# Kernel optimization log

Hardware: AMD Instinct MI355X
Metric: run time of the kernel (lower is better)

Reference implementation:

```python
import jax, jax.numpy as jnp
import numpy as np

B, T_ENC, U = 8, 200, 100
VOCAB, ENC_DIM, PRED_DIM, EMBED_DIM = 1024, 512, 512, 128


def setup_inputs() -> dict:
    key = jax.random.key(0)
    ks = jax.random.split(key, 13)
    n = lambda k, shape, fan_in: (jax.random.normal(k, shape, jnp.float32) / np.sqrt(fan_in)).astype(jnp.float32)
    return {
        "enc_out": jax.random.normal(ks[0], (B, T_ENC, ENC_DIM), jnp.float32),
        "targets": jax.random.randint(ks[1], (B, U), 0, VOCAB, jnp.int32),
        "target_len": jnp.full((B,), U, jnp.int32),
        # params
        "emb_table": n(ks[2], (VOCAB + 1, EMBED_DIM), 1.0),
        "W_ih": n(ks[3], (4 * PRED_DIM, EMBED_DIM), EMBED_DIM),
        "W_hh": n(ks[4], (4 * PRED_DIM, PRED_DIM), PRED_DIM),
        "b_ih": jnp.zeros((4 * PRED_DIM,), jnp.float32),
        "b_hh": jnp.zeros((4 * PRED_DIM,), jnp.float32),
        "W_enc": n(ks[5], (PRED_DIM, ENC_DIM), ENC_DIM),
        "b_enc": jnp.zeros((PRED_DIM,), jnp.float32),
        "W_pred": n(ks[6], (PRED_DIM, PRED_DIM), PRED_DIM),
        "b_pred": jnp.zeros((PRED_DIM,), jnp.float32),
        "W_joint": n(ks[7], (VOCAB + 1, PRED_DIM), PRED_DIM),
        "b_joint": jnp.zeros((VOCAB + 1,), jnp.float32),
    }


def reference(enc_out, targets, target_len, emb_table, W_ih, W_hh, b_ih, b_hh,
              W_enc, b_enc, W_pred, b_pred, W_joint, b_joint):
    # targets_with_blank: prepend blank_id = vocab_size
    blank_id = emb_table.shape[0] - 1
    Bsz = targets.shape[0]
    tw = jnp.concatenate([jnp.full((Bsz, 1), blank_id, targets.dtype), targets], axis=1)
    emb = emb_table[tw]  # (B, U+1, E)

    P = W_hh.shape[1]
    h0 = jnp.zeros((Bsz, P), emb.dtype)

    def lstm_step(carry, x_t):
        h, c = carry
        gates = x_t @ W_ih.T + b_ih + h @ W_hh.T + b_hh  # (B, 4P)
        i, f, g, o = jnp.split(gates, 4, axis=-1)  # PyTorch LSTMCell gate order
        i, f, o = jax.nn.sigmoid(i), jax.nn.sigmoid(f), jax.nn.sigmoid(o)
        c = f * c + i * jnp.tanh(g)
        h = o * jnp.tanh(c)
        return (h, c), h

    _, pred = jax.lax.scan(lstm_step, (h0, h0), jnp.swapaxes(emb, 0, 1))
    pred = jnp.swapaxes(pred, 0, 1)  # (B, U+1, P)

    f_enc = enc_out @ W_enc.T + b_enc   # (B, T, P)
    f_pred = pred @ W_pred.T + b_pred   # (B, U+1, P)
    joint = jnp.tanh(f_enc[:, :, None, :] + f_pred[:, None, :, :])  # (B, T, U+1, P)
    logits = joint @ W_joint.T + b_joint  # (B, T, U+1, V+1)
    return logits
```

## Files before the change

kernel.cpp:

```cpp
#include <hip/hip_runtime.h>
#include <stdint.h>
#include <stddef.h>

#define BB 8
#define TENC 200
#define UU 100
#define UP1 101
#define VP1 1025
#define ED 128
#define PD 512
#define LSTM_NWG 64

typedef __attribute__((ext_vector_type(8))) unsigned short ushort8;
typedef __attribute__((ext_vector_type(8))) __bf16 bf16x8;
typedef __attribute__((ext_vector_type(4))) float f32x4;

__device__ __forceinline__ float bf2f(unsigned short u){
  unsigned int x = ((unsigned int)u) << 16;
  return __builtin_bit_cast(float, x);
}
__device__ __forceinline__ unsigned short f2bf(float f){
  unsigned int x = __builtin_bit_cast(unsigned int, f);
  unsigned int r = (x + 0x7fffu + ((x >> 16) & 1u)) >> 16;
  return (unsigned short)r;
}
__device__ __forceinline__ float tanh_fast(float x){
  float e = __expf(2.0f * x);
  return 1.0f - 2.0f / (e + 1.0f);
}
__device__ __forceinline__ float sigm(float x){
  return 1.0f / (1.0f + __expf(-x));
}
__device__ __forceinline__ void gload_lds16(const unsigned short* gsrc, unsigned short* ldst){
  __builtin_amdgcn_global_load_lds((const __attribute__((address_space(1))) void*)gsrc,
                                   (__attribute__((address_space(3))) void*)ldst, 16, 0, 0);
}

__global__ __launch_bounds__(256) void k_cvt_bf16(const float* __restrict__ src,
                                                  unsigned short* __restrict__ dst, int n){
  int i = blockIdx.x * 256 + threadIdx.x;
  if (i < n) dst[i] = f2bf(src[i]);
}

__global__ __launch_bounds__(256) void k_xgate(
    const float* __restrict__ emb, const int* __restrict__ targets,
    const float* __restrict__ W_ih, const float* __restrict__ b_ih,
    const float* __restrict__ b_hh, float* __restrict__ xg)
{
  __shared__ float e_s[BB * ED];
  const int u  = blockIdx.x >> 2;
  const int jq = blockIdx.x & 3;
  const int tid = threadIdx.x;
  for (int idx = tid; idx < BB * ED; idx += 256){
    int b = idx >> 7, e = idx & 127;
    int tok = (u == 0) ? 1024 : targets[b * UU + (u - 1)];
    e_s[idx] = emb[(size_t)tok * ED + e];
  }
  __syncthreads();
  float acc[2][BB];
  #pragma unroll
  for (int r = 0; r < 2; r++)
    #pragma unroll
    for (int b = 0; b < BB; b++) acc[r][b] = 0.0f;
  const int j0 = jq * 512 + tid;
  const float* w0p = W_ih + (size_t)j0 * ED;
  const float* w1p = W_ih + (size_t)(j0 + 256) * ED;
  for (int e = 0; e < ED; e++){
    float w0 = w0p[e], w1 = w1p[e];
    #pragma unroll
    for (int b = 0; b < BB; b++){
      float ev = e_s[b * ED + e];
      acc[0][b] = fmaf(ev, w0, acc[0][b]);
      acc[1][b] = fmaf(ev, w1, acc[1][b]);
    }
  }
  #pragma unroll
  for (int r = 0; r < 2; r++){
    int j = j0 + r * 256;
    float bias = b_ih[j] + b_hh[j];
    #pragma unroll
    for (int b = 0; b < BB; b++)
      xg[((size_t)b * UP1 + u) * 2048 + j] = acc[r][b] + bias;
  }
}

__global__ __launch_bounds__(256) void k_lstm_all(
    const float* __restrict__ xg, const float* __restrict__ W_hh,
    float* __restrict__ pred, unsigned int* __restrict__ cnt)
{
  __shared__ float h_s[8][520];
  __shared__ float red[32 * 257];
  __shared__ float gates_s[32][9];
  const int tid = threadIdx.x;
  const int wg  = blockIdx.x;
  const int p0  = wg * 8;
  const int jg = tid >> 5, kc = tid & 31;
  const float* wrow[4];
  #pragma unroll
  for (int r = 0; r < 4; r++){
    int jl = jg * 4 + r;
    int grow = (jl >> 3) * PD + p0 + (jl & 7);
    wrow[r] = W_hh + (size_t)grow * PD;
  }
  float c_reg = 0.0f;
  for (int u = 0; u < UP1; u++){
    float xi = 0.f, xf = 0.f, xgv = 0.f, xo = 0.f;
    if (tid < 64){
      int pl = tid >> 3, b = tid & 7;
      const float* xr = xg + ((size_t)(b * UP1 + u)) * 2048;
      int p = p0 + pl;
      xi = xr[p]; xf = xr[512 + p]; xgv = xr[1024 + p]; xo = xr[1536 + p];
    }
    if (u > 0){
      if (tid == 0){
        while (__hip_atomic_load(&cnt[u - 1], __ATOMIC_RELAXED, __HIP_MEMORY_SCOPE_AGENT) < LSTM_NWG)
          __builtin_amdgcn_s_sleep(8);
      }
      __syncthreads();
      float tmp[16];
      #pragma unroll
      for (int j = 0; j < 16; j++){
        int i = tid + 256 * j;
        int b2 = i >> 9, k = i & 511;
        tmp[j] = __hip_atomic_load(pred + ((size_t)(b2 * UP1 + (u - 1))) * PD + k,
                                   __ATOMIC_RELAXED, __HIP_MEMORY_SCOPE_AGENT);
      }
      #pragma unroll
      for (int j = 0; j < 16; j++){
        int i = tid + 256 * j;
        h_s[i >> 9][i & 511] = tmp[j];
      }
    } else {
      for (int i = tid; i < 8 * PD; i += 256) h_s[i >> 9][i & 511] = 0.0f;
    }
    __syncthreads();
    float acc[4][BB];
    #pragma unroll
    for (int r = 0; r < 4; r++)
      #pragma unroll
      for (int b = 0; b < BB; b++) acc[r][b] = 0.0f;
    for (int i = 0; i < 16; i++){
      int k = kc + 32 * i;
      float hv[BB];
      #pragma unroll
      for (int b = 0; b < BB; b++) hv[b] = h_s[b][k];
      #pragma unroll
      for (int r = 0; r < 4; r++){
        float wv = wrow[r][k];
        #pragma unroll
        for (int b = 0; b < BB; b++) acc[r][b] = fmaf(hv[b], wv, acc[r][b]);
      }
    }
    #pragma unroll
    for (int r = 0; r < 4; r++)
      #pragma unroll
      for (int b = 0; b < BB; b++)
        red[kc * 257 + jg * 32 + r * 8 + b] = acc[r][b];
    __syncthreads();
    {
      int jl = tid >> 3, b = tid & 7;
      float s = 0.0f;
      #pragma unroll
      for (int kk = 0; kk < 32; kk++)
        s += red[kk * 257 + (jl >> 2) * 32 + (jl & 3) * 8 + b];
      gates_s[jl][b] = s;
    }
    __syncthreads();
    if (tid < 64){
      int pl = tid >> 3, b = tid & 7;
      int p = p0 + pl;
      float gi = gates_s[0  + pl][b] + xi;
      float gf = gates_s[8  + pl][b] + xf;
      float gg = gates_s[16 + pl][b] + xgv;
      float go = gates_s[24 + pl][b] + xo;
      float iv = sigm(gi), fv = sigm(gf), ov = sigm(go);
      c_reg = fv * c_reg + iv * tanh_fast(gg);
      float hval = ov * tanh_fast(c_reg);
      __hip_atomic_store(pred + ((size_t)(b * UP1 + u)) * PD + p, hval,
                         __ATOMIC_RELAXED, __HIP_MEMORY_SCOPE_AGENT);
    }
    if (u < UP1 - 1){
      if (tid == 0){
        asm volatile("s_waitcnt vmcnt(0)" ::: "memory");
        __hip_atomic_fetch_add(&cnt[u], 1u, __ATOMIC_RELAXED, __HIP_MEMORY_SCOPE_AGENT);
      }
    }
  }
}

__global__ __launch_bounds__(256) void k_gemm_bias_bf16(
    const float* __restrict__ A, const float* __restrict__ W,
    const float* __restrict__ bias, unsigned short* __restrict__ out, int M)
{
  __shared__ float a_s[16][68];
  __shared__ float b_s[16][68];
  const int m0 = blockIdx.x * 64, n0 = blockIdx.y * 64;
  const int tid = threadIdx.x;
  const int tx = tid & 15, ty = tid >> 4;
  float acc[4][4];
  #pragma unroll
  for (int i2 = 0; i2 < 4; i2++)
    #pragma unroll
    for (int j2 = 0; j2 < 4; j2++) acc[i2][j2] = 0.0f;
  for (int k0 = 0; k0 < 512; k0 += 16){
    int mm = tid >> 2, k4 = (tid & 3) * 4;
    int row = m0 + mm; if (row >= M) row = M - 1;
    float4 av = *(const float4*)(A + (size_t)row * 512 + k0 + k4);
    a_s[k4 + 0][mm] = av.x; a_s[k4 + 1][mm] = av.y;
    a_s[k4 + 2][mm] = av.z; a_s[k4 + 3][mm] = av.w;
    float4 bv = *(const float4*)(W + (size_t)(n0 + mm) * 512 + k0 + k4);
    b_s[k4 + 0][mm] = bv.x; b_s[k4 + 1][mm] = bv.y;
    b_s[k4 + 2][mm] = bv.z; b_s[k4 + 3][mm] = bv.w;
    __syncthreads();
    #pragma unroll
    for (int k = 0; k < 16; k++){
      float4 a4 = *(const float4*)&a_s[k][ty * 4];
      float4 b4 = *(const float4*)&b_s[k][tx * 4];
      float aa[4] = {a4.x, a4.y, a4.z, a4.w};
      float bb[4] = {b4.x, b4.y, b4.z, b4.w};
      #pragma unroll
      for (int i2 = 0; i2 < 4; i2++)
        #pragma unroll
        for (int j2 = 0; j2 < 4; j2++)
          acc[i2][j2] = fmaf(aa[i2], bb[j2], acc[i2][j2]);
    }
    __syncthreads();
  }
  #pragma unroll
  for (int i2 = 0; i2 < 4; i2++){
    int m = m0 + ty * 4 + i2;
    if (m < M){
      #pragma unroll
      for (int j2 = 0; j2 < 4; j2++){
        int n = n0 + tx * 4 + j2;
        out[(size_t)m * 512 + n] = f2bf(acc[i2][j2] + bias[n]);
      }
    }
  }
}

__global__ __launch_bounds__(512, 1) void k_joint3(
    const unsigned short* __restrict__ fe, const unsigned short* __restrict__ fp,
    const unsigned short* __restrict__ wj, const float* __restrict__ bj,
    float* __restrict__ out)
{
  __shared__ unsigned short A_s[128 * 512];
  __shared__ unsigned short B_s[3][128 * 32];
  const int tu = blockIdx.x;
  const int b  = blockIdx.y;
  const int tt = tu / 13, ut = tu - tt * 13;
  const int t0 = tt * 16, u0 = ut * 8;
  const int tid = threadIdx.x;
  const int w = tid >> 6, l = tid & 63;
  const int l15 = l & 15, lg = l >> 4;
  const int wr = w >> 1, wc = w & 1;

  auto issue = [&](int idx){
    int nt = idx >> 4, ks = idx & 15;
    int rb = tid >> 2, cs = tid & 3;
    int col8 = cs ^ ((rb >> 1) & 3);
    const unsigned short* src = wj + (size_t)(nt * 128 + rb) * 512 + ks * 32 + col8 * 8;
    gload_lds16(src, (unsigned short*)B_s[idx % 3] + (size_t)(w * 64) * 8);
  };

  issue(0);

  for (int rr = 0; rr < 16; rr++){
    int row = rr * 8 + w;
    int ti = row >> 3, ui = row & 7;
    int t = t0 + ti, uu = u0 + ui;
    ushort8 a = {0,0,0,0,0,0,0,0};
    if (t < TENC && uu < UP1){
      ushort8 f8 = *(const ushort8*)(fe + (size_t)(b * TENC + t) * 512 + l * 8);
      ushort8 p8 = *(const ushort8*)(fp + (size_t)(b * UP1 + uu) * 512 + l * 8);
      #pragma unroll
      for (int j = 0; j < 8; j++)
        a[j] = f2bf(tanh_fast(bf2f(f8[j]) + bf2f(p8[j])));
    }
    int byteo = row * 1024 + ((l * 16) ^ ((row & 7) << 4));
    *(ushort8*)((char*)A_s + byteo) = a;
  }
  __syncthreads();

  f32x4 acc[2][4];
  #pragma unroll
  for (int fr = 0; fr < 2; fr++)
    #pragma unroll
    for (int fc = 0; fc < 4; fc++)
      acc[fr][fc] = (f32x4){0.f, 0.f, 0.f, 0.f};

  for (int idx = 0; idx < 128; idx++){
    const int nt = idx >> 4, ks = idx & 15;
    if (idx + 1 < 128){
      issue(idx + 1);
      asm volatile("s_waitcnt vmcnt(1)" ::: "memory");
    } else {
      asm volatile("s_waitcnt vmcnt(0)" ::: "memory");
    }
    __builtin_amdgcn_s_barrier();

    const unsigned short* bb = (const unsigned short*)B_s[idx % 3];
    bf16x8 bfr[4], afr[2];
    #pragma unroll
    for (int fc = 0; fc < 4; fc++){
      int rb = wc * 64 + fc * 16 + l15;
      int byteo = rb * 64 + ((lg ^ ((rb >> 1) & 3)) * 16);
      bfr[fc] = __builtin_bit_cast(bf16x8, *(const ushort8*)((const char*)bb + byteo));
    }
    #pragma unroll
    for (int fr = 0; fr < 2; fr++){
      int ra = wr * 32 + fr * 16 + l15;
      int k8 = ks * 4 + lg;
      int byteo = ra * 1024 + ((k8 * 16) ^ ((ra & 7) << 4));
      afr[fr] = __builtin_bit_cast(bf16x8, *(const ushort8*)((const char*)A_s + byteo));
    }
    #pragma unroll
    for (int fr = 0; fr < 2; fr++)
      #pragma unroll
      for (int fc = 0; fc < 4; fc++)
        acc[fr][fc] = __builtin_amdgcn_mfma_f32_16x16x32_bf16(bfr[fc], afr[fr], acc[fr][fc], 0, 0, 0);

    if (ks == 15){
      #pragma unroll
      for (int fr = 0; fr < 2; fr++){
        int m = wr * 32 + fr * 16 + l15;
        int t = t0 + (m >> 3), uu2 = u0 + (m & 7);
        if (t < TENC && uu2 < UP1){
          float* orow = out + ((size_t)(b * TENC + t) * UP1 + uu2) * VP1;
          #pragma unroll
          for (int fc = 0; fc < 4; fc++){
            int nb = nt * 128 + wc * 64 + fc * 16 + lg * 4;
            float4 bv = *(const float4*)(bj + nb);
            f32x4 v = acc[fr][fc];
            float4 st = {v[0] + bv.x, v[1] + bv.y, v[2] + bv.z, v[3] + bv.w};
            *(float4*)(orow + nb) = st;
          }
        }
        #pragma unroll
        for (int fc = 0; fc < 4; fc++)
          acc[fr][fc] = (f32x4){0.f, 0.f, 0.f, 0.f};
      }
    }
  }

  {
    int row = tid >> 2, q = tid & 3;
    float s = 0.0f;
    const unsigned short* w1 = wj + (size_t)1024 * 512;
    #pragma unroll 4
    for (int j = 0; j < 16; j++){
      int k8 = q * 16 + j;
      int byteo = row * 1024 + ((k8 * 16) ^ ((row & 7) << 4));
      ushort8 a8 = *(const ushort8*)((const char*)A_s + byteo);
      ushort8 w8 = *(const ushort8*)(w1 + k8 * 8);
      #pragma unroll
      for (int jj = 0; jj < 8; jj++)
        s += bf2f(a8[jj]) * bf2f(w8[jj]);
    }
    s += __shfl_xor(s, 1);
    s += __shfl_xor(s, 2);
    if (q == 0){
      int t = t0 + (row >> 3), uu = u0 + (row & 7);
      if (t < TENC && uu < UP1)
        out[((size_t)(b * TENC + t) * UP1 + uu) * VP1 + 1024] = s + bj[1024];
    }
  }
}

extern "C" void kernel_launch(void* const* d_in, const int* in_sizes, int n_in,
                              void* d_out, int out_size, void* d_ws, size_t ws_size,
                              hipStream_t stream) {
  const float* enc_out = (const float*)d_in[0];
  const int*   targets = (const int*)d_in[1];
  const float* emb     = (const float*)d_in[3];
  const float* W_ih    = (const float*)d_in[4];
  const float* W_hh    = (const float*)d_in[5];
  const float* b_ih    = (const float*)d_in[6];
  const float* b_hh    = (const float*)d_in[7];
  const float* W_enc   = (const float*)d_in[8];
  const float* b_enc   = (const float*)d_in[9];
  const float* W_pred  = (const float*)d_in[10];
  const float* b_pred  = (const float*)d_in[11];
  const float* W_joint = (const float*)d_in[12];
  const float* b_joint = (const float*)d_in[13];
  float* out = (float*)d_out;

  char* ws = (char*)d_ws;
  float* xg            = (float*)(ws + 0);
  float* pred          = (float*)(ws + 6619136);
  unsigned short* feb  = (unsigned short*)(ws + 8273920);
  unsigned short* fpb  = (unsigned short*)(ws + 9912320);
  unsigned short* wjb  = (unsigned short*)(ws + 10739712);
  unsigned int*   cnt  = (unsigned int*)(ws + 11789312);

  hipMemsetAsync(cnt, 0, UP1 * sizeof(unsigned int), stream);
  hipLaunchKernelGGL(k_cvt_bf16, dim3((VP1 * 512 + 255) / 256), dim3(256), 0, stream,
                     W_joint, wjb, VP1 * 512);
  hipLaunchKernelGGL(k_xgate, dim3(404), dim3(256), 0, stream,
                     emb, targets, W_ih, b_ih, b_hh, xg);
  hipLaunchKernelGGL(k_gemm_bias_bf16, dim3(25, 8), dim3(256), 0, stream,
                     enc_out, W_enc, b_enc, feb, 1600);
  hipLaunchKernelGGL(k_lstm_all, dim3(LSTM_NWG), dim3(256), 0, stream,
                     xg, W_hh, pred, cnt);
  hipLaunchKernelGGL(k_gemm_bias_bf16, dim3(13, 8), dim3(256), 0, stream,
                     pred, W_pred, b_pred, fpb, 808);
  hipLaunchKernelGGL(k_joint3, dim3(169, 8), dim3(512), 0, stream,
                     feb, fpb, wjb, b_joint, out);
}
```

Before: 1.004 ms.

## Cache LSTM weights in LDS, per-WG flag sync, deeper joint prefetch, nontemporal stores

The persistent LSTM kernel now loads its W_hh slice into LDS once and computes each gate/batch dot product per thread, which removes the cross-thread reduction. Grid sync changes from one shared atomic counter to per-workgroup sequence flags polled by a wavefront. The hidden state is exchanged through a small double-buffered array read with cache-bypassing loads. The joint GEMM prefetches two B tiles ahead with a single barrier per step and writes logits with nontemporal stores. The added LDS use and the more aggressive polling could raise occupancy or contention costs.

```diff
diff --git a/kernel.cpp b/kernel.cpp
--- a/kernel.cpp
+++ b/kernel.cpp
@@ -86,104 +86,90 @@
 
 __global__ __launch_bounds__(256) void k_lstm_all(
     const float* __restrict__ xg, const float* __restrict__ W_hh,
-    float* __restrict__ pred, unsigned int* __restrict__ cnt)
+    float* __restrict__ pred, float* __restrict__ hb, unsigned int* __restrict__ seq)
 {
+  __shared__ float W_s[32][520];
   __shared__ float h_s[8][520];
-  __shared__ float red[32 * 257];
-  __shared__ float gates_s[32][9];
+  __shared__ float gates_s[32][8];
   const int tid = threadIdx.x;
   const int wg  = blockIdx.x;
   const int p0  = wg * 8;
-  const int jg = tid >> 5, kc = tid & 31;
-  const float* wrow[4];
-  #pragma unroll
-  for (int r = 0; r < 4; r++){
-    int jl = jg * 4 + r;
-    int grow = (jl >> 3) * PD + p0 + (jl & 7);
-    wrow[r] = W_hh + (size_t)grow * PD;
+  const int row = tid >> 3, bb = tid & 7;
+  {
+    int r = tid >> 3;
+    int grow = (r >> 3) * PD + p0 + (r & 7);
+    const float* src = W_hh + (size_t)grow * PD;
+    for (int c = (tid & 7); c < 128; c += 8)
+      *(float4*)&W_s[r][c * 4] = *(const float4*)(src + c * 4);
   }
   float c_reg = 0.0f;
+  __syncthreads();
   for (int u = 0; u < UP1; u++){
-    float xi = 0.f, xf = 0.f, xgv = 0.f, xo = 0.f;
-    if (tid < 64){
-      int pl = tid >> 3, b = tid & 7;
-      const float* xr = xg + ((size_t)(b * UP1 + u)) * 2048;
-      int p = p0 + pl;
-      xi = xr[p]; xf = xr[512 + p]; xgv = xr[1024 + p]; xo = xr[1536 + p];
-    }
+    float xv = xg[((size_t)(bb * UP1 + u)) * 2048 + (row >> 3) * 512 + p0 + (row & 7)];
     if (u > 0){
-      if (tid == 0){
-        while (__hip_atomic_load(&cnt[u - 1], __ATOMIC_RELAXED, __HIP_MEMORY_SCOPE_AGENT) < LSTM_NWG)
-          __builtin_amdgcn_s_sleep(8);
+      if (tid < 64){
+        while (1){
+          unsigned int v = __hip_atomic_load(&seq[tid], __ATOMIC_RELAXED, __HIP_MEMORY_SCOPE_AGENT);
+          if (__all(v >= (unsigned int)u)) break;
+          __builtin_amdgcn_s_sleep(1);
+        }
       }
       __syncthreads();
-      float tmp[16];
-      #pragma unroll
-      for (int j = 0; j < 16; j++){
-        int i = tid + 256 * j;
-        int b2 = i >> 9, k = i & 511;
-        tmp[j] = __hip_atomic_load(pred + ((size_t)(b2 * UP1 + (u - 1))) * PD + k,
-                                   __ATOMIC_RELAXED, __HIP_MEMORY_SCOPE_AGENT);
-      }
-      #pragma unroll
-      for (int j = 0; j < 16; j++){
-        int i = tid + 256 * j;
-        h_s[i >> 9][i & 511] = tmp[j];
-      }
+      const float* hsrc = hb + ((u - 1) & 1) * 4096 + tid * 16;
+      float4 t0, t1, t2, t3;
+      asm volatile("global_load_dwordx4 %0, %4, off sc0 sc1\n\t"
+                   "global_load_dwordx4 %1, %5, off sc0 sc1\n\t"
+                   "global_load_dwordx4 %2, %6, off sc0 sc1\n\t"
+                   "global_load_dwordx4 %3, %7, off sc0 sc1\n\t"
+                   "s_waitcnt vmcnt(0)"
+                   : "=&v"(t0), "=&v"(t1), "=&v"(t2), "=&v"(t3)
+                   : "v"(hsrc), "v"(hsrc + 4), "v"(hsrc + 8), "v"(hsrc + 12)
+                   : "memory");
+      int hb2 = tid >> 5, hk = (tid & 31) * 16;
+      *(float4*)&h_s[hb2][hk]      = t0;
+      *(float4*)&h_s[hb2][hk + 4]  = t1;
+      *(float4*)&h_s[hb2][hk + 8]  = t2;
+      *(float4*)&h_s[hb2][hk + 12] = t3;
+      __syncthreads();
     } else {
       for (int i = tid; i < 8 * PD; i += 256) h_s[i >> 9][i & 511] = 0.0f;
-    }
-    __syncthreads();
-    float acc[4][BB];
-    #pragma unroll
-    for (int r = 0; r < 4; r++)
-      #pragma unroll
-      for (int b = 0; b < BB; b++) acc[r][b] = 0.0f;
-    for (int i = 0; i < 16; i++){
-      int k = kc + 32 * i;
-      float hv[BB];
-      #pragma unroll
-      for (int b = 0; b < BB; b++) hv[b] = h_s[b][k];
-      #pragma unroll
-      for (int r = 0; r < 4; r++){
-        float wv = wrow[r][k];
-        #pragma unroll
-        for (int b = 0; b < BB; b++) acc[r][b] = fmaf(hv[b], wv, acc[r][b]);
-      }
-    }
-    #pragma unroll
-    for (int r = 0; r < 4; r++)
-      #pragma unroll
-      for (int b = 0; b < BB; b++)
-        red[kc * 257 + jg * 32 + r * 8 + b] = acc[r][b];
-    __syncthreads();
-    {
-      int jl = tid >> 3, b = tid & 7;
-      float s = 0.0f;
-      #pragma unroll
-      for (int kk = 0; kk < 32; kk++)
-        s += red[kk * 257 + (jl >> 2) * 32 + (jl & 3) * 8 + b];
-      gates_s[jl][b] = s;
-    }
+      __syncthreads();
+    }
+    float a0 = 0.f, a1 = 0.f, a2 = 0.f, a3 = 0.f;
+    #pragma unroll 4
+    for (int k = 0; k < PD; k += 16){
+      float4 w0 = *(const float4*)&W_s[row][k],      h0 = *(const float4*)&h_s[bb][k];
+      float4 w1 = *(const float4*)&W_s[row][k + 4],  h1 = *(const float4*)&h_s[bb][k + 4];
+      float4 w2 = *(const float4*)&W_s[row][k + 8],  h2 = *(const float4*)&h_s[bb][k + 8];
+      float4 w3 = *(const float4*)&W_s[row][k + 12], h3 = *(const float4*)&h_s[bb][k + 12];
+      a0 = fmaf(w0.x, h0.x, a0); a0 = fmaf(w0.y, h0.y, a0);
+      a0 = fmaf(w0.z, h0.z, a0); a0 = fmaf(w0.w, h0.w, a0);
+      a1 = fmaf(w1.x, h1.x, a1); a1 = fmaf(w1.y, h1.y, a1);
+      a1 = fmaf(w1.z, h1.z, a1); a1 = fmaf(w1.w, h1.w, a1);
+      a2 = fmaf(w2.x, h2.x, a2); a2 = fmaf(w2.y, h2.y, a2);
+      a2 = fmaf(w2.z, h2.z, a2); a2 = fmaf(w2.w, h2.w, a2);
+      a3 = fmaf(w3.x, h3.x, a3); a3 = fmaf(w3.y, h3.y, a3);
+      a3 = fmaf(w3.z, h3.z, a3); a3 = fmaf(w3.w, h3.w, a3);
+    }
+    gates_s[row][bb] = a0 + a1 + a2 + a3 + xv;
     __syncthreads();
     if (tid < 64){
-      int pl = tid >> 3, b = tid & 7;
-      int p = p0 + pl;
-      float gi = gates_s[0  + pl][b] + xi;
-      float gf = gates_s[8  + pl][b] + xf;
-      float gg = gates_s[16 + pl][b] + xgv;
-      float go = gates_s[24 + pl][b] + xo;
+      int pl = tid >> 3, b2 = tid & 7;
+      float gi = gates_s[pl][b2];
+      float gf = gates_s[8  + pl][b2];
+      float gg = gates_s[16 + pl][b2];
+      float go = gates_s[24 + pl][b2];
       float iv = sigm(gi), fv = sigm(gf), ov = sigm(go);
       c_reg = fv * c_reg + iv * tanh_fast(gg);
       float hval = ov * tanh_fast(c_reg);
-      __hip_atomic_store(pred + ((size_t)(b * UP1 + u)) * PD + p, hval,
+      __hip_atomic_store(hb + (u & 1) * 4096 + b2 * 512 + p0 + pl, hval,
                          __ATOMIC_RELAXED, __HIP_MEMORY_SCOPE_AGENT);
-    }
-    if (u < UP1 - 1){
-      if (tid == 0){
-        asm volatile("s_waitcnt vmcnt(0)" ::: "memory");
-        __hip_atomic_fetch_add(&cnt[u], 1u, __ATOMIC_RELAXED, __HIP_MEMORY_SCOPE_AGENT);
-      }
+      pred[((size_t)(b2 * UP1 + u)) * PD + p0 + pl] = hval;
+    }
+    if (u < UP1 - 1 && tid == 0){
+      asm volatile("s_waitcnt vmcnt(0)" ::: "memory");
+      __hip_atomic_store(&seq[wg], (unsigned int)(u + 1),
+                         __ATOMIC_RELAXED, __HIP_MEMORY_SCOPE_AGENT);
     }
   }
 }
@@ -239,7 +225,7 @@
   }
 }
 
-__global__ __launch_bounds__(512, 1) void k_joint3(
+__global__ __launch_bounds__(512, 1) void k_joint4(
     const unsigned short* __restrict__ fe, const unsigned short* __restrict__ fp,
     const unsigned short* __restrict__ wj, const float* __restrict__ bj,
     float* __restrict__ out)
@@ -263,7 +249,7 @@
     gload_lds16(src, (unsigned short*)B_s[idx % 3] + (size_t)(w * 64) * 8);
   };
 
-  issue(0);
+  issue(0); issue(1);
 
   for (int rr = 0; rr < 16; rr++){
     int row = rr * 8 + w;
@@ -291,21 +277,19 @@
 
   for (int idx = 0; idx < 128; idx++){
     const int nt = idx >> 4, ks = idx & 15;
-    if (idx + 1 < 128){
-      issue(idx + 1);
+    if (idx > 0){
       asm volatile("s_waitcnt vmcnt(1)" ::: "memory");
-    } else {
-      asm volatile("s_waitcnt vmcnt(0)" ::: "memory");
-    }
-    __builtin_amdgcn_s_barrier();
-
-    const unsigned short* bb = (const unsigned short*)B_s[idx % 3];
+      __builtin_amdgcn_s_barrier();
+    }
+    if (idx + 2 < 128) issue(idx + 2);
+
+    const unsigned short* bbuf = (const unsigned short*)B_s[idx % 3];
     bf16x8 bfr[4], afr[2];
     #pragma unroll
     for (int fc = 0; fc < 4; fc++){
       int rb = wc * 64 + fc * 16 + l15;
       int byteo = rb * 64 + ((lg ^ ((rb >> 1) & 3)) * 16);
-      bfr[fc] = __builtin_bit_cast(bf16x8, *(const ushort8*)((const char*)bb + byteo));
+      bfr[fc] = __builtin_bit_cast(bf16x8, *(const ushort8*)((const char*)bbuf + byteo));
     }
     #pragma unroll
     for (int fr = 0; fr < 2; fr++){
@@ -332,8 +316,8 @@
             int nb = nt * 128 + wc * 64 + fc * 16 + lg * 4;
             float4 bv = *(const float4*)(bj + nb);
             f32x4 v = acc[fr][fc];
-            float4 st = {v[0] + bv.x, v[1] + bv.y, v[2] + bv.z, v[3] + bv.w};
-            *(float4*)(orow + nb) = st;
+            f32x4 st = {v[0] + bv.x, v[1] + bv.y, v[2] + bv.z, v[3] + bv.w};
+            __builtin_nontemporal_store(st, (f32x4*)(orow + nb));
           }
         }
         #pragma unroll
@@ -391,9 +375,10 @@
   unsigned short* feb  = (unsigned short*)(ws + 8273920);
   unsigned short* fpb  = (unsigned short*)(ws + 9912320);
   unsigned short* wjb  = (unsigned short*)(ws + 10739712);
-  unsigned int*   cnt  = (unsigned int*)(ws + 11789312);
-
-  hipMemsetAsync(cnt, 0, UP1 * sizeof(unsigned int), stream);
+  float* hb            = (float*)(ws + 11789312);
+  unsigned int* seq    = (unsigned int*)(ws + 11822080);
+
+  (void)hipMemsetAsync(seq, 0, LSTM_NWG * sizeof(unsigned int), stream);
   hipLaunchKernelGGL(k_cvt_bf16, dim3((VP1 * 512 + 255) / 256), dim3(256), 0, stream,
                      W_joint, wjb, VP1 * 512);
   hipLaunchKernelGGL(k_xgate, dim3(404), dim3(256), 0, stream,
@@ -401,9 +386,9 @@
   hipLaunchKernelGGL(k_gemm_bias_bf16, dim3(25, 8), dim3(256), 0, stream,
                      enc_out, W_enc, b_enc, feb, 1600);
   hipLaunchKernelGGL(k_lstm_all, dim3(LSTM_NWG), dim3(256), 0, stream,
-                     xg, W_hh, pred, cnt);
+                     xg, W_hh, pred, hb, seq);
   hipLaunchKernelGGL(k_gemm_bias_bf16, dim3(13, 8), dim3(256), 0, stream,
                      pred, W_pred, b_pred, fpb, 808);
-  hipLaunchKernelGGL(k_joint3, dim3(169, 8), dim3(512), 0, stream,
+  hipLaunchKernelGGL(k_joint4, dim3(169, 8), dim3(512), 0, stream,
                      feb, fpb, wjb, b_joint, out);
 }
```

After: 1.342 ms. +33.7%, slower.
